# Performance work log

Hardware: AMD Instinct MI355X
Metric: run time of the kernel (lower is better)

The kernel has to match this reference:

```python
import jax, jax.numpy as jnp
import numpy as np

B, S, D = 2, 2048, 1024
H = 16
HD = D // H  # 64

def setup_inputs() -> dict:
    key = jax.random.key(0)
    ks = jax.random.split(key, 6)
    scale = 0.02
    return {
        "query": jax.random.normal(ks[0], (B, S, D), dtype=jnp.float32),
        "key":   jax.random.normal(ks[1], (B, S, D), dtype=jnp.float32),
        "value": jax.random.normal(ks[2], (B, S, D), dtype=jnp.float32),
        "Wq": jax.random.normal(ks[3], (D, D), dtype=jnp.float32) * scale,
        "bq": jnp.zeros((D,), dtype=jnp.float32),
        "Wk": jax.random.normal(ks[4], (D, D), dtype=jnp.float32) * scale,
        "bk": jnp.zeros((D,), dtype=jnp.float32),
        "Wv": jax.random.normal(ks[5], (D, D), dtype=jnp.float32) * scale,
        "bv": jnp.zeros((D,), dtype=jnp.float32),
    }

def reference(query, key, value, Wq, bq, Wk, bk, Wv, bv):
    b, s, d = query.shape
    # Linear projections (weights stored as (in, out))
    q = query @ Wq + bq   # [B,S,D]
    k = key   @ Wk + bk
    v = value @ Wv + bv
    # split heads -> [B,H,S,HD]
    q = q.reshape(b, s, H, HD).transpose(0, 2, 1, 3)
    k = k.reshape(b, s, H, HD).transpose(0, 2, 1, 3)
    v = v.reshape(b, s, H, HD).transpose(0, 2, 1, 3)
    # scaled dot-product attention (no mask; dropout = identity in eval)
    scores = jnp.einsum("bhqd,bhkd->bhqk", q, k) / jnp.sqrt(jnp.float32(HD))
    attn = jax.nn.softmax(scores, axis=-1)
    out = jnp.einsum("bhqk,bhkd->bhqd", attn, v)
    # merge heads -> [B,S,D]
    return out.transpose(0, 2, 1, 3).reshape(b, s, d)
```

## Files before the change

### kernel.cpp

```cpp
#include <hip/hip_runtime.h>
#include <stdint.h>

#define D_  1024
#define S_  2048
#define B_  2
#define H_  16
#define HD_ 64
#define M_  (B_*S_)
#define KVB 64

typedef unsigned short u16;
typedef __attribute__((ext_vector_type(8)))  __bf16 bf16x8;
typedef __attribute__((ext_vector_type(4)))  float  f32x4;
typedef __attribute__((ext_vector_type(16))) float  f32x16;

__device__ __forceinline__ u16 f2bf(float f) {
    __bf16 h = (__bf16)f;
    union { __bf16 h; u16 u; } x; x.h = h;
    return x.u;
}

__device__ __forceinline__ void gload_lds16(const void* g, void* l) {
    __builtin_amdgcn_global_load_lds(
        (const __attribute__((address_space(1))) uint32_t*)g,
        (__attribute__((address_space(3))) uint32_t*)l, 16, 0, 0);
}

__global__ __launch_bounds__(256) void cvt3_kernel(
    const float* __restrict__ a, const float* __restrict__ b, const float* __restrict__ c,
    u16* __restrict__ oa, u16* __restrict__ ob, u16* __restrict__ oc) {
    const float* in = blockIdx.y == 0 ? a : (blockIdx.y == 1 ? b : c);
    u16* out = blockIdx.y == 0 ? oa : (blockIdx.y == 1 ? ob : oc);
    int i = (blockIdx.x * 256 + threadIdx.x) * 4;
    float4 v = *(const float4*)(in + i);
    ushort4 o;
    o.x = f2bf(v.x); o.y = f2bf(v.y); o.z = f2bf(v.z); o.w = f2bf(v.w);
    *(ushort4*)(out + i) = o;
}

__global__ __launch_bounds__(256) void transpose_w3(
    const float* __restrict__ Wq, const float* __restrict__ Wk, const float* __restrict__ Wv,
    u16* __restrict__ Wtq, u16* __restrict__ Wtk, u16* __restrict__ Wtv) {
    const float* W = blockIdx.z == 0 ? Wq : (blockIdx.z == 1 ? Wk : Wv);
    u16* Wt = blockIdx.z == 0 ? Wtq : (blockIdx.z == 1 ? Wtk : Wtv);
    __shared__ u16 t[64][65];
    int k0 = blockIdx.x * 64, n0 = blockIdx.y * 64;
    int tid = threadIdx.x;
    int c4 = (tid & 15) * 4, r = tid >> 4;
#pragma unroll
    for (int i = 0; i < 4; i++) {
        int row = r + i * 16;
        float4 v = *(const float4*)(W + (uint64_t)(k0 + row) * D_ + n0 + c4);
        t[row][c4 + 0] = f2bf(v.x);
        t[row][c4 + 1] = f2bf(v.y);
        t[row][c4 + 2] = f2bf(v.z);
        t[row][c4 + 3] = f2bf(v.w);
    }
    __syncthreads();
#pragma unroll
    for (int i = 0; i < 4; i++) {
        int nrow = r + i * 16;
        ushort4 o;
        o.x = t[c4 + 0][nrow]; o.y = t[c4 + 1][nrow];
        o.z = t[c4 + 2][nrow]; o.w = t[c4 + 3][nrow];
        *(ushort4*)(Wt + (uint64_t)(n0 + nrow) * D_ + k0 + c4) = o;
    }
}

__global__ __launch_bounds__(256) void gemm_qkv(
    const u16* __restrict__ Xq, const u16* __restrict__ Xk, const u16* __restrict__ Xv,
    const u16* __restrict__ Wtq, const u16* __restrict__ Wtk, const u16* __restrict__ Wtv,
    const float* __restrict__ bq, const float* __restrict__ bk, const float* __restrict__ bv,
    u16* __restrict__ Qo, u16* __restrict__ Ko, u16* __restrict__ Vo)
{
    int p = blockIdx.z;
    const u16* X    = p == 0 ? Xq  : (p == 1 ? Xk  : Xv);
    const u16* Wt   = p == 0 ? Wtq : (p == 1 ? Wtk : Wtv);
    const float* bias = p == 0 ? bq : (p == 1 ? bk : bv);
    u16* out = p == 0 ? Qo : (p == 1 ? Ko : Vo);
    float scale = p == 0 ? 0.125f : 1.0f;

    __shared__ __align__(16) u16 As[3][64 * 32];
    __shared__ __align__(16) u16 Bs[3][128 * 32];

    int tid = threadIdx.x;
    int lane = tid & 63, wid = tid >> 6;
    int lrow = lane & 15, lk = lane >> 4;
    int wr = wid >> 1, wc = wid & 1;
    int bm = blockIdx.x, bn = blockIdx.y;

    f32x4 acc[2][4] = {};

    const uint64_t Xrow0 = (uint64_t)bm * 64 * D_;
    const uint64_t Wrow0 = (uint64_t)bn * 128 * D_;

    auto stage = [&](int buf, int kt) {
        int k0 = kt * 32;
        {
            int row = tid >> 2;
            int cg = (tid & 3) ^ ((row >> 1) & 3);
            gload_lds16(X + Xrow0 + (uint64_t)row * D_ + k0 + cg * 8,
                        (char*)As[buf] + wid * 1024);
        }
#pragma unroll
        for (int it = 0; it < 2; ++it) {
            int i = it * 256 + tid;
            int row = i >> 2;
            int cg = (i & 3) ^ ((row >> 1) & 3);
            gload_lds16(Wt + Wrow0 + (uint64_t)row * D_ + k0 + cg * 8,
                        (char*)Bs[buf] + it * 4096 + wid * 1024);
        }
    };

    stage(0, 0);
    stage(1, 1);
    asm volatile("s_waitcnt vmcnt(3)" ::: "memory");
    __builtin_amdgcn_s_barrier();

    const int NKT = D_ / 32;
    for (int kt = 0; kt < NKT; ++kt) {
        int cur = kt % 3;
        if (kt + 2 < NKT) stage((kt + 2) % 3, kt + 2);

        bf16x8 a[2], b[4];
#pragma unroll
        for (int m = 0; m < 2; m++) {
            int r = wr * 32 + m * 16 + lrow;
            a[m] = *(const bf16x8*)((const char*)As[cur] + r * 64 + ((lk ^ ((r >> 1) & 3)) * 16));
        }
#pragma unroll
        for (int n = 0; n < 4; n++) {
            int r = wc * 64 + n * 16 + lrow;
            b[n] = *(const bf16x8*)((const char*)Bs[cur] + r * 64 + ((lk ^ ((r >> 1) & 3)) * 16));
        }
        if (p < 2) {
#pragma unroll
            for (int m = 0; m < 2; m++)
#pragma unroll
                for (int n = 0; n < 4; n++)
                    acc[m][n] = __builtin_amdgcn_mfma_f32_16x16x32_bf16(a[m], b[n], acc[m][n], 0, 0, 0);
        } else {
#pragma unroll
            for (int m = 0; m < 2; m++)
#pragma unroll
                for (int n = 0; n < 4; n++)
                    acc[m][n] = __builtin_amdgcn_mfma_f32_16x16x32_bf16(b[n], a[m], acc[m][n], 0, 0, 0);
        }

        if (kt + 1 < NKT) {
            if (kt + 2 < NKT)
                asm volatile("s_waitcnt vmcnt(3)" ::: "memory");
            else
                asm volatile("s_waitcnt vmcnt(0)" ::: "memory");
            __builtin_amdgcn_s_barrier();
        }
    }

    if (p < 2) {
#pragma unroll
        for (int m = 0; m < 2; m++) {
            int grow_base = bm * 64 + wr * 32 + m * 16 + lk * 4;
#pragma unroll
            for (int n = 0; n < 4; n++) {
                int gcol = bn * 128 + wc * 64 + n * 16 + lrow;
                float bb = bias[gcol];
                int h = gcol >> 6, hd = gcol & 63;
#pragma unroll
                for (int j = 0; j < 4; j++) {
                    int grow = grow_base + j;
                    int b_ = grow >> 11, s = grow & 2047;
                    out[(((uint64_t)(b_ * H_ + h)) * S_ + s) * HD_ + hd] =
                        f2bf((acc[m][n][j] + bb) * scale);
                }
            }
        }
    } else {
#pragma unroll
        for (int m = 0; m < 2; m++) {
            int sg = bm * 64 + wr * 32 + m * 16 + lrow;
            int b_ = sg >> 11, s = sg & 2047;
#pragma unroll
            for (int n = 0; n < 4; n++) {
                int ch_base = bn * 128 + wc * 64 + n * 16 + lk * 4;
#pragma unroll
                for (int j = 0; j < 4; j++) {
                    int ch = ch_base + j;
                    int h = ch >> 6, hd = ch & 63;
                    out[(((uint64_t)(b_ * H_ + h)) * HD_ + hd) * S_ + s] =
                        f2bf(acc[m][n][j] + bias[ch]);
                }
            }
        }
    }
}

__global__ __launch_bounds__(512) void attn_kernel(
    const u16* __restrict__ Q, const u16* __restrict__ K,
    const u16* __restrict__ VT, float* __restrict__ out)
{
    __shared__ __align__(16) char smem[32768];

    int lin = blockIdx.x;
    int bh = lin & 31, qt = lin >> 5;

    int tid = threadIdx.x;
    int w = tid >> 6, lane = tid & 63;
    int q5 = lane & 31, h = lane >> 5;

    bf16x8 qf[4];
    const u16* Qrow = Q + ((uint64_t)bh * S_ + qt * 256 + w * 32 + q5) * HD_;
#pragma unroll
    for (int kk = 0; kk < 4; kk++)
        qf[kk] = *(const bf16x8*)(Qrow + kk * 16 + h * 8);

    f32x16 o_acc[2] = {};
    float m_run = -1e30f, l_run = 0.f;

    const char* Kbase = (const char*)(K  + (uint64_t)bh * S_ * HD_);
    const char* Vbase = (const char*)(VT + (uint64_t)bh * HD_ * S_);

    int o16 = tid * 16;
    int rr  = o16 >> 7;
    int os  = o16 ^ ((rr & 7) << 4);

    auto stage = [&](int buf, int t) {
        int kv0 = t * KVB;
        gload_lds16(Kbase + (uint64_t)kv0 * 128 + os,
                    smem + buf * 8192 + w * 1024);
        gload_lds16(Vbase + (uint64_t)rr * (S_ * 2) + kv0 * 2 + (os & 127),
                    smem + 16384 + buf * 8192 + w * 1024);
    };

    stage(0, 0);
    __syncthreads();
    int cur = 0;

    const int NT = S_ / KVB;
    for (int t = 0; t < NT; ++t) {
        if (t + 1 < NT) stage(cur ^ 1, t + 1);

        const char* Kc = smem + cur * 8192;
        const char* Vc = smem + 16384 + cur * 8192;
        int sw = (q5 & 7) << 4;

        f32x16 sacc[2] = {};
        __builtin_amdgcn_s_setprio(1);
#pragma unroll
        for (int c = 0; c < 2; c++) {
            int rb = (c * 32 + q5) * 128;
#pragma unroll
            for (int kk = 0; kk < 4; kk++) {
                bf16x8 kf = *(const bf16x8*)(Kc + rb + ((kk * 32 + h * 16) ^ sw));
                sacc[c] = __builtin_amdgcn_mfma_f32_32x32x16_bf16(kf, qf[kk], sacc[c], 0, 0, 0);
            }
        }
        __builtin_amdgcn_s_setprio(0);

        float mp = sacc[0][0];
#pragma unroll
        for (int r = 1; r < 16; r++) mp = fmaxf(mp, sacc[0][r]);
#pragma unroll
        for (int r = 0; r < 16; r++) mp = fmaxf(mp, sacc[1][r]);
        mp = fmaxf(mp, __shfl_xor(mp, 32, 64));
        float mnew = fmaxf(m_run, mp);
        float sc = __expf(m_run - mnew);
        m_run = mnew;

        float ts = 0.f;
#pragma unroll
        for (int c = 0; c < 2; c++)
#pragma unroll
            for (int r = 0; r < 16; r++) {
                float pv = __expf(sacc[c][r] - mnew);
                sacc[c][r] = pv;
                ts += pv;
            }
        ts += __shfl_xor(ts, 32, 64);
        l_run = l_run * sc + ts;
#pragma unroll
        for (int hb = 0; hb < 2; hb++)
#pragma unroll
            for (int r = 0; r < 16; r++) o_acc[hb][r] *= sc;

        bf16x8 pa[4];
#pragma unroll
        for (int ks = 0; ks < 4; ks++) {
            int c = ks >> 1, gg = ks & 1;
            uint32_t a0, a1, b0, b1;
            asm("v_cvt_pk_bf16_f32 %0, %1, %2" : "=v"(a0) : "v"(sacc[c][8*gg+0]), "v"(sacc[c][8*gg+1]));
            asm("v_cvt_pk_bf16_f32 %0, %1, %2" : "=v"(a1) : "v"(sacc[c][8*gg+2]), "v"(sacc[c][8*gg+3]));
            asm("v_cvt_pk_bf16_f32 %0, %1, %2" : "=v"(b0) : "v"(sacc[c][8*gg+4]), "v"(sacc[c][8*gg+5]));
            asm("v_cvt_pk_bf16_f32 %0, %1, %2" : "=v"(b1) : "v"(sacc[c][8*gg+6]), "v"(sacc[c][8*gg+7]));
            asm volatile("v_permlane32_swap_b32 %0, %1" : "+v"(a0), "+v"(b0));
            asm volatile("v_permlane32_swap_b32 %0, %1" : "+v"(a1), "+v"(b1));
            union { uint32_t u[4]; bf16x8 v; } pu;
            pu.u[0] = a0; pu.u[1] = a1; pu.u[2] = b0; pu.u[3] = b1;
            pa[ks] = pu.v;
        }

        __builtin_amdgcn_s_setprio(1);
#pragma unroll
        for (int hb = 0; hb < 2; hb++) {
            int rb = (hb * 32 + q5) * 128;
#pragma unroll
            for (int ks = 0; ks < 4; ks++) {
                bf16x8 vf = *(const bf16x8*)(Vc + rb + ((ks * 32 + h * 16) ^ sw));
                o_acc[hb] = __builtin_amdgcn_mfma_f32_32x32x16_bf16(vf, pa[ks], o_acc[hb], 0, 0, 0);
            }
        }
        __builtin_amdgcn_s_setprio(0);

        __syncthreads();
        cur ^= 1;
    }

    float inv = 1.0f / l_run;
    int b_ = bh >> 4, head = bh & 15;
    int qq = lane >> 1, c0 = (lane & 1) * 16;
    float* scrw = (float*)smem + w * 1024;
    float* orow = out + ((uint64_t)(b_ * S_ + qt * 256 + w * 32 + qq)) * D_ + head * 64;
#pragma unroll
    for (int hb = 0; hb < 2; hb++) {
#pragma unroll
        for (int r = 0; r < 16; r++) {
            int col = (r & 3) + 8 * (r >> 2) + 4 * h;
            scrw[q5 * 32 + (col ^ ((q5 & 7) << 2))] = o_acc[hb][r] * inv;
        }
        __syncthreads();
#pragma unroll
        for (int j = 0; j < 4; j++) {
            int cb = c0 + j * 4;
            float4 val = *(float4*)&scrw[qq * 32 + (cb ^ ((qq & 7) << 2))];
            *(float4*)(orow + hb * 32 + cb) = val;
        }
        __syncthreads();
    }
}

extern "C" void kernel_launch(void* const* d_in, const int* in_sizes, int n_in,
                              void* d_out, int out_size, void* d_ws, size_t ws_size,
                              hipStream_t stream) {
    const float* q  = (const float*)d_in[0];
    const float* k  = (const float*)d_in[1];
    const float* v  = (const float*)d_in[2];
    const float* Wq = (const float*)d_in[3];
    const float* bq = (const float*)d_in[4];
    const float* Wk = (const float*)d_in[5];
    const float* bk = (const float*)d_in[6];
    const float* Wv = (const float*)d_in[7];
    const float* bv = (const float*)d_in[8];
    float* out = (float*)d_out;

    u16* ws = (u16*)d_ws;
    const size_t XN = (size_t)M_ * D_;
    const size_t WN = (size_t)D_ * D_;
    u16* Xq  = ws;          u16* Xk  = Xq  + XN;  u16* Xv  = Xk  + XN;
    u16* Wtq = Xv + XN;     u16* Wtk = Wtq + WN;  u16* Wtv = Wtk + WN;
    u16* Qb  = Wtv + WN;    u16* Kb  = Qb  + XN;  u16* Vb  = Kb  + XN;

    cvt3_kernel<<<dim3(XN / 1024, 3), 256, 0, stream>>>(q, k, v, Xq, Xk, Xv);
    transpose_w3<<<dim3(16, 16, 3), 256, 0, stream>>>(Wq, Wk, Wv, Wtq, Wtk, Wtv);
    gemm_qkv<<<dim3(64, 8, 3), 256, 0, stream>>>(Xq, Xk, Xv, Wtq, Wtk, Wtv,
                                                 bq, bk, bv, Qb, Kb, Vb);
    attn_kernel<<<256, 512, 0, stream>>>(Qb, Kb, Vb, out);
}
```

Measured before the change: 214.6 us.

## Merge prep kernels and split attention into smaller 128-query blocks with swizzle

```diff
diff --git a/kernel.cpp b/kernel.cpp
--- a/kernel.cpp
+++ b/kernel.cpp
@@ -26,44 +26,51 @@
         (__attribute__((address_space(3))) uint32_t*)l, 16, 0, 0);
 }
 
-__global__ __launch_bounds__(256) void cvt3_kernel(
-    const float* __restrict__ a, const float* __restrict__ b, const float* __restrict__ c,
-    u16* __restrict__ oa, u16* __restrict__ ob, u16* __restrict__ oc) {
-    const float* in = blockIdx.y == 0 ? a : (blockIdx.y == 1 ? b : c);
-    u16* out = blockIdx.y == 0 ? oa : (blockIdx.y == 1 ? ob : oc);
-    int i = (blockIdx.x * 256 + threadIdx.x) * 4;
-    float4 v = *(const float4*)(in + i);
-    ushort4 o;
-    o.x = f2bf(v.x); o.y = f2bf(v.y); o.z = f2bf(v.z); o.w = f2bf(v.w);
-    *(ushort4*)(out + i) = o;
-}
-
-__global__ __launch_bounds__(256) void transpose_w3(
+__global__ __launch_bounds__(256) void prep_kernel(
+    const float* __restrict__ q, const float* __restrict__ k, const float* __restrict__ v,
+    u16* __restrict__ Xq, u16* __restrict__ Xk, u16* __restrict__ Xv,
     const float* __restrict__ Wq, const float* __restrict__ Wk, const float* __restrict__ Wv,
-    u16* __restrict__ Wtq, u16* __restrict__ Wtk, u16* __restrict__ Wtv) {
-    const float* W = blockIdx.z == 0 ? Wq : (blockIdx.z == 1 ? Wk : Wv);
-    u16* Wt = blockIdx.z == 0 ? Wtq : (blockIdx.z == 1 ? Wtk : Wtv);
+    u16* __restrict__ Wtq, u16* __restrict__ Wtk, u16* __restrict__ Wtv)
+{
     __shared__ u16 t[64][65];
-    int k0 = blockIdx.x * 64, n0 = blockIdx.y * 64;
-    int tid = threadIdx.x;
-    int c4 = (tid & 15) * 4, r = tid >> 4;
-#pragma unroll
-    for (int i = 0; i < 4; i++) {
-        int row = r + i * 16;
-        float4 v = *(const float4*)(W + (uint64_t)(k0 + row) * D_ + n0 + c4);
-        t[row][c4 + 0] = f2bf(v.x);
-        t[row][c4 + 1] = f2bf(v.y);
-        t[row][c4 + 2] = f2bf(v.z);
-        t[row][c4 + 3] = f2bf(v.w);
-    }
-    __syncthreads();
-#pragma unroll
-    for (int i = 0; i < 4; i++) {
-        int nrow = r + i * 16;
+    int bid = blockIdx.x;
+    if (bid < 12288) {
+        int sl = bid >> 12;
+        int bx = bid & 4095;
+        const float* in = sl == 0 ? q : (sl == 1 ? k : v);
+        u16* out = sl == 0 ? Xq : (sl == 1 ? Xk : Xv);
+        int i = (bx * 256 + threadIdx.x) * 4;
+        float4 vv = *(const float4*)(in + i);
         ushort4 o;
-        o.x = t[c4 + 0][nrow]; o.y = t[c4 + 1][nrow];
-        o.z = t[c4 + 2][nrow]; o.w = t[c4 + 3][nrow];
-        *(ushort4*)(Wt + (uint64_t)(n0 + nrow) * D_ + k0 + c4) = o;
+        o.x = f2bf(vv.x); o.y = f2bf(vv.y); o.z = f2bf(vv.z); o.w = f2bf(vv.w);
+        *(ushort4*)(out + i) = o;
+    } else {
+        int tt = bid - 12288;
+        int z = tt >> 8;
+        int rem = tt & 255;
+        const float* W = z == 0 ? Wq : (z == 1 ? Wk : Wv);
+        u16* Wt = z == 0 ? Wtq : (z == 1 ? Wtk : Wtv);
+        int k0 = (rem & 15) * 64, n0 = (rem >> 4) * 64;
+        int tid = threadIdx.x;
+        int c4 = (tid & 15) * 4, r = tid >> 4;
+#pragma unroll
+        for (int i = 0; i < 4; i++) {
+            int row = r + i * 16;
+            float4 vv = *(const float4*)(W + (uint64_t)(k0 + row) * D_ + n0 + c4);
+            t[row][c4 + 0] = f2bf(vv.x);
+            t[row][c4 + 1] = f2bf(vv.y);
+            t[row][c4 + 2] = f2bf(vv.z);
+            t[row][c4 + 3] = f2bf(vv.w);
+        }
+        __syncthreads();
+#pragma unroll
+        for (int i = 0; i < 4; i++) {
+            int nrow = r + i * 16;
+            ushort4 o;
+            o.x = t[c4 + 0][nrow]; o.y = t[c4 + 1][nrow];
+            o.z = t[c4 + 2][nrow]; o.w = t[c4 + 3][nrow];
+            *(ushort4*)(Wt + (uint64_t)(n0 + nrow) * D_ + k0 + c4) = o;
+        }
     }
 }
 
@@ -194,21 +201,22 @@
     }
 }
 
-__global__ __launch_bounds__(512) void attn_kernel(
+__global__ __launch_bounds__(256) void attn_kernel(
     const u16* __restrict__ Q, const u16* __restrict__ K,
     const u16* __restrict__ VT, float* __restrict__ out)
 {
     __shared__ __align__(16) char smem[32768];
 
     int lin = blockIdx.x;
-    int bh = lin & 31, qt = lin >> 5;
+    int swz = (lin & 7) * 64 + (lin >> 3);
+    int qt = swz & 15, bh = swz >> 4;
 
     int tid = threadIdx.x;
     int w = tid >> 6, lane = tid & 63;
     int q5 = lane & 31, h = lane >> 5;
 
     bf16x8 qf[4];
-    const u16* Qrow = Q + ((uint64_t)bh * S_ + qt * 256 + w * 32 + q5) * HD_;
+    const u16* Qrow = Q + ((uint64_t)bh * S_ + qt * 128 + w * 32 + q5) * HD_;
 #pragma unroll
     for (int kk = 0; kk < 4; kk++)
         qf[kk] = *(const bf16x8*)(Qrow + kk * 16 + h * 8);
@@ -219,16 +227,19 @@
     const char* Kbase = (const char*)(K  + (uint64_t)bh * S_ * HD_);
     const char* Vbase = (const char*)(VT + (uint64_t)bh * HD_ * S_);
 
-    int o16 = tid * 16;
-    int rr  = o16 >> 7;
-    int os  = o16 ^ ((rr & 7) << 4);
-
     auto stage = [&](int buf, int t) {
         int kv0 = t * KVB;
-        gload_lds16(Kbase + (uint64_t)kv0 * 128 + os,
-                    smem + buf * 8192 + w * 1024);
-        gload_lds16(Vbase + (uint64_t)rr * (S_ * 2) + kv0 * 2 + (os & 127),
-                    smem + 16384 + buf * 8192 + w * 1024);
+#pragma unroll
+        for (int it = 0; it < 2; ++it) {
+            int i = it * 256 + tid;
+            int o = i * 16;
+            int rr = o >> 7;
+            int os = o ^ ((rr & 7) << 4);
+            gload_lds16(Kbase + (uint64_t)kv0 * 128 + os,
+                        smem + buf * 8192 + it * 4096 + w * 1024);
+            gload_lds16(Vbase + (uint64_t)rr * (S_ * 2) + kv0 * 2 + (os & 127),
+                        smem + 16384 + buf * 8192 + it * 4096 + w * 1024);
+        }
     };
 
     stage(0, 0);
@@ -318,7 +329,7 @@
     int b_ = bh >> 4, head = bh & 15;
     int qq = lane >> 1, c0 = (lane & 1) * 16;
     float* scrw = (float*)smem + w * 1024;
-    float* orow = out + ((uint64_t)(b_ * S_ + qt * 256 + w * 32 + qq)) * D_ + head * 64;
+    float* orow = out + ((uint64_t)(b_ * S_ + qt * 128 + w * 32 + qq)) * D_ + head * 64;
 #pragma unroll
     for (int hb = 0; hb < 2; hb++) {
 #pragma unroll
@@ -358,9 +369,9 @@
     u16* Wtq = Xv + XN;     u16* Wtk = Wtq + WN;  u16* Wtv = Wtk + WN;
     u16* Qb  = Wtv + WN;    u16* Kb  = Qb  + XN;  u16* Vb  = Kb  + XN;
 
-    cvt3_kernel<<<dim3(XN / 1024, 3), 256, 0, stream>>>(q, k, v, Xq, Xk, Xv);
-    transpose_w3<<<dim3(16, 16, 3), 256, 0, stream>>>(Wq, Wk, Wv, Wtq, Wtk, Wtv);
+    prep_kernel<<<13056, 256, 0, stream>>>(q, k, v, Xq, Xk, Xv,
+                                           Wq, Wk, Wv, Wtq, Wtk, Wtv);
     gemm_qkv<<<dim3(64, 8, 3), 256, 0, stream>>>(Xq, Xk, Xv, Wtq, Wtk, Wtv,
                                                  bq, bk, bv, Qb, Kb, Vb);
-    attn_kernel<<<256, 512, 0, stream>>>(Qb, Kb, Vb, out);
-}
+    attn_kernel<<<512, 256, 0, stream>>>(Qb, Kb, Vb, out);
+}
```

Measured after the change: 219.1 us. 2.1% more time.
